# Optimization experiments

Measured on AMD Instinct MI355X. Metric: run time of the kernel, lower is better.

Reference implementation:

```python
import jax, jax.numpy as jnp
import numpy as np

B, T, D, DI, K, M, H, HD, L, VOCAB = 8, 512, 256, 512, 4, 2, 4, 64, 2, 272


def rmsnorm(x, w, eps=1e-6):
    return x * jax.lax.rsqrt(jnp.mean(x * x, axis=-1, keepdims=True) + eps) * w


def rotate_half(x):
    x1, x2 = x[..., ::2], x[..., 1::2]
    return jnp.stack([-x2, x1], axis=-1).reshape(x.shape)


def causal_conv(x, w, b):
    # x: [B,T,C], w: [C,K] depthwise causal conv, then silu
    y = jax.lax.conv_general_dilated(
        x.transpose(0, 2, 1), w[:, None, :],
        window_strides=(1,), padding=[(K - 1, 0)],
        feature_group_count=x.shape[-1])
    return jax.nn.silu(y.transpose(0, 2, 1) + b)


def delta_memory(x, Wv, Wg, Wb, Wa, A_log, dt_bias, Wblend, Wout):
    # x: [B,T,D]; per-timestep delta-rule fast-weight update with decay + key rotation
    Bv, Tn, Dm = x.shape
    vals = (x @ Wv).reshape(Bv, Tn, M, H, HD)
    gate = jax.nn.sigmoid(x @ Wg)                                   # [B,T,H]
    beta = jax.nn.sigmoid(jnp.einsum('btd,mdh->btmh', x, Wb))       # [B,T,M,H]
    alpha = jnp.einsum('btd,mdh->btmh', x, Wa) + dt_bias            # [B,T,M,H]
    decay = jnp.exp(-jnp.exp(A_log)[None, None] * jax.nn.softplus(alpha))
    blend = jax.nn.softmax((x @ Wblend).reshape(Bv, Tn, H, M), axis=-1)
    rk0 = x.reshape(Bv, Tn, H, HD)
    rk0 = rk0 / jnp.maximum(jnp.linalg.norm(rk0, axis=-1, keepdims=True), 1e-12)
    rks = [rk0]
    for _ in range(M - 1):
        rks.append(rotate_half(rks[-1]))
    rks = jnp.stack(rks, axis=2)                                    # [B,T,M,H,d]
    wks = jnp.pad(rks[:, :-1], ((0, 0), (1, 0), (0, 0), (0, 0), (0, 0)))  # shifted keys

    def step(S, inp):
        v, wk, rk, bt, dc, bl, g = inp
        S = S * dc[..., None, None]                                  # [B,M,H,d,d]
        pred = jnp.einsum('bmhdk,bmhd->bmhk', S, wk)
        err = (v - pred) * bt[..., None]
        S = S + wk[..., None] * err[..., None, :]                    # outer-product write
        read = jnp.einsum('bmhdk,bmhd->bmhk', S, rk)
        o = jnp.einsum('bhm,bmhk->bhk', bl, read) * g[..., None]
        return S, o

    tf = lambda a: jnp.moveaxis(a, 1, 0)
    xs = (tf(vals), tf(wks), tf(rks), tf(beta), tf(decay), tf(blend), tf(gate))
    S0 = jnp.zeros((Bv, M, H, HD, HD), x.dtype)
    _, o = jax.lax.scan(step, S0, xs)                                # [T,B,H,d]
    o = jnp.moveaxis(o, 0, 1).reshape(Bv, Tn, Dm)
    return x + o @ Wout


def setup_inputs():
    key = jax.random.key(0)
    ks = jax.random.split(key, 16)
    n = lambda k, shape, sc=0.02: jax.random.normal(k, shape, jnp.float32) * sc
    return {
        'ids': jax.random.randint(ks[0], (B, T), 0, VOCAB, jnp.int32),
        'emb': n(ks[1], (VOCAB, D)),
        'norm_w': jnp.ones((L, D), jnp.float32),
        'W_up': n(ks[2], (L, D, DI)),
        'W_gate': n(ks[3], (L, D, DI)),
        'W_down': n(ks[4], (L, DI, D)),
        'conv_w': n(ks[5], (L, DI, K), 0.1),
        'conv_b': jnp.zeros((L, DI), jnp.float32),
        'Wv': n(ks[6], (L, D, M * D)),
        'Wg': n(ks[7], (L, D, H)),
        'Wb': n(ks[8], (L, M, D, H)),
        'Wa': n(ks[9], (L, M, D, H)),
        'A_log': n(ks[10], (L, M, H), 0.5),
        'dt_bias': n(ks[11], (L, M, H), 0.5),
        'Wblend': n(ks[12], (L, D, H * M)),
        'Wout': n(ks[13], (L, D, D)),
        'final_norm_w': jnp.ones((D,), jnp.float32),
    }


def reference(ids, emb, norm_w, W_up, W_gate, W_down, conv_w, conv_b,
              Wv, Wg, Wb, Wa, A_log, dt_bias, Wblend, Wout, final_norm_w):
    x = emb[ids]
    for l in range(L):
        nx = rmsnorm(x, norm_w[l])
        h = causal_conv(nx @ W_up[l], conv_w[l], conv_b[l])
        out = (jax.nn.silu(nx @ W_gate[l]) * h) @ W_down[l]
        out = delta_memory(out, Wv[l], Wg[l], Wb[l], Wa[l],
                           A_log[l], dt_bias[l], Wblend[l], Wout[l])
        x = x + out
    return rmsnorm(x, final_norm_w) @ emb.T  # tied head
```

## Files before the change

### kernel.cpp

```cpp
#include <hip/hip_runtime.h>
#include <math.h>

#define BB 8
#define TT 512
#define DD 256
#define DIM 512
#define KW 4
#define MM 2
#define HH 4
#define HDIM 64
#define LL 2
#define VV 272

typedef __attribute__((ext_vector_type(8))) short bf16x8;
typedef __attribute__((ext_vector_type(4))) float f32x4;

__device__ __forceinline__ float sigf(float x){ return 1.f/(1.f+__expf(-x)); }
__device__ __forceinline__ float siluf(float x){ return x/(1.f+__expf(-x)); }

__device__ __forceinline__ unsigned short f2bf(float f){
  unsigned int u = __float_as_uint(f);
  unsigned int r = (u + 0x7FFFu + ((u >> 16) & 1u)) >> 16;
  return (unsigned short)r;
}
__device__ __forceinline__ float bf2f(unsigned short s){
  return __uint_as_float(((unsigned int)s) << 16);
}

__device__ __forceinline__ float xor1_add(float x){
  int y = __builtin_amdgcn_update_dpp(0, __float_as_int(x), 0xB1, 0xF, 0xF, true);
  return x + __int_as_float(y);
}
__device__ __forceinline__ float xor2_add(float x){
  int y = __builtin_amdgcn_update_dpp(0, __float_as_int(x), 0x4E, 0xF, 0xF, true);
  return x + __int_as_float(y);
}
__device__ __forceinline__ float xor8_add(float x){
  int y = __builtin_amdgcn_update_dpp(0, __float_as_int(x), 0x128, 0xF, 0xF, true);
  return x + __int_as_float(y);
}
__device__ __forceinline__ float ror4_add(float x){
  int y = __builtin_amdgcn_update_dpp(0, __float_as_int(x), 0x124, 0xF, 0xF, true);
  return x + __int_as_float(y);
}
__device__ __forceinline__ float ror8_add(float x){
  int y = __builtin_amdgcn_update_dpp(0, __float_as_int(x), 0x128, 0xF, 0xF, true);
  return x + __int_as_float(y);
}

__device__ __forceinline__ void gl_lds16(const void* g, void* l){
  __builtin_amdgcn_global_load_lds(
      (const __attribute__((address_space(1))) unsigned int*)g,
      (__attribute__((address_space(3))) unsigned int*)l,
      16, 0, 0);
}

#define LWB 589824
__global__ void k_cvt(const float* __restrict__ Wup, const float* __restrict__ Wgate,
                      const float* __restrict__ Wdown, const float* __restrict__ Wv,
                      const float* __restrict__ Wout, const float* __restrict__ emb,
                      unsigned short* __restrict__ wbf){
  int idx = blockIdx.x*256 + threadIdx.x;
  if (idx >= 2*LWB + VV*DD) return;
  float v;
  if (idx < 2*LWB){
    int l = (idx >= LWB) ? 1 : 0;
    int local = idx - l*LWB;
    if (local < 131072){ int n = local>>8, k = local&255;
      v = Wup[(size_t)l*131072 + k*DIM + n]; }
    else if (local < 262144){ local -= 131072; int n = local>>8, k = local&255;
      v = Wgate[(size_t)l*131072 + k*DIM + n]; }
    else if (local < 393216){ local -= 262144; int n = local>>9, k = local&511;
      v = Wdown[(size_t)l*131072 + k*DD + n]; }
    else if (local < 524288){ local -= 393216; int n = local>>8, k = local&255;
      v = Wv[(size_t)l*131072 + k*DIM + n]; }
    else { local -= 524288; int n = local>>8, k = local&255;
      v = Wout[(size_t)l*65536 + k*DD + n]; }
  } else {
    v = emb[idx - 2*LWB];
  }
  wbf[idx] = f2bf(v);
}

__global__ void k_embed(const int* __restrict__ ids, const float* __restrict__ emb,
                        float* __restrict__ x){
  int row = blockIdx.x;
  int d = threadIdx.x;
  x[row*DD + d] = emb[ids[row]*DD + d];
}

__global__ void k_rmsnorm(const float* __restrict__ in, const float* __restrict__ w,
                          unsigned short* __restrict__ out){
  int row = blockIdx.x;
  int l = threadIdx.x;
  float4 v = *(const float4*)&in[row*DD + l*4];
  float ss = v.x*v.x + v.y*v.y + v.z*v.z + v.w*v.w;
  #pragma unroll
  for (int o = 32; o > 0; o >>= 1) ss += __shfl_xor(ss, o, 64);
  float sc = rsqrtf(ss*(1.f/DD) + 1e-6f);
  float4 wv = *(const float4*)&w[l*4];
  ushort4 r;
  r.x = f2bf(v.x*sc*wv.x); r.y = f2bf(v.y*sc*wv.y);
  r.z = f2bf(v.z*sc*wv.z); r.w = f2bf(v.w*sc*wv.w);
  *(ushort4*)&out[row*DD + l*4] = r;
}

template<int MODE>
__global__ void __launch_bounds__(256) k_gemm2(const unsigned short* __restrict__ A,
                                               const unsigned short* __restrict__ Bt,
                                               float* __restrict__ Cf,
                                               unsigned short* __restrict__ Cb,
                                               int N, int K){
  __shared__ unsigned short as[64][72];
  __shared__ unsigned short bs[64][72];
  const int tid = threadIdx.x;
  const int w = tid >> 6, l = tid & 63;
  const int m0 = blockIdx.y*64, n0 = blockIdx.x*64;
  const int ar = tid >> 2, ac = (tid & 3)*16;
  f32x4 acc[4] = {};
  for (int k0 = 0; k0 < K; k0 += 64){
    { const bf16x8* src = (const bf16x8*)&A[(size_t)(m0+ar)*K + k0 + ac];
      *(bf16x8*)&as[ar][ac]   = src[0];
      *(bf16x8*)&as[ar][ac+8] = src[1];
    }
    { int n = n0 + ar;
      bf16x8 z; z = (bf16x8)(short)0;
      bf16x8 b0 = z, b1 = z;
      if (n < N){
        const bf16x8* src = (const bf16x8*)&Bt[(size_t)n*K + k0 + ac];
        b0 = src[0]; b1 = src[1];
      }
      *(bf16x8*)&bs[ar][ac]   = b0;
      *(bf16x8*)&bs[ar][ac+8] = b1;
    }
    __syncthreads();
    const int mr = w*16 + (l & 15);
    const int kb = (l >> 4)*8;
    #pragma unroll
    for (int kc2 = 0; kc2 < 2; ++kc2){
      bf16x8 af = *(const bf16x8*)&as[mr][kc2*32 + kb];
      #pragma unroll
      for (int nt = 0; nt < 4; ++nt){
        bf16x8 bfr = *(const bf16x8*)&bs[nt*16 + (l & 15)][kc2*32 + kb];
        acc[nt] = __builtin_amdgcn_mfma_f32_16x16x32_bf16(af, bfr, acc[nt], 0, 0, 0);
      }
    }
    __syncthreads();
  }
  #pragma unroll
  for (int nt = 0; nt < 4; ++nt){
    int col = n0 + nt*16 + (l & 15);
    if (col < N){
      #pragma unroll
      for (int r = 0; r < 4; ++r){
        int row = m0 + w*16 + (l >> 4)*4 + r;
        if (MODE == 0 || MODE == 2) Cf[(size_t)row*N + col] = acc[nt][r];
        if (MODE == 1 || MODE == 2) Cb[(size_t)row*N + col] = f2bf(acc[nt][r]);
      }
    }
  }
}

__global__ void __launch_bounds__(256) k_gemm_up(const unsigned short* __restrict__ A,
                                                 const unsigned short* __restrict__ But,
                                                 const unsigned short* __restrict__ Bgt,
                                                 unsigned short* __restrict__ Cu,
                                                 unsigned short* __restrict__ Cg){
  __shared__ unsigned short as[64][72];
  __shared__ unsigned short bu[64][72];
  __shared__ unsigned short bg[64][72];
  const int tid = threadIdx.x;
  const int w = tid >> 6, l = tid & 63;
  const int m0 = blockIdx.y*64, n0 = blockIdx.x*64;
  const int ar = tid >> 2, ac = (tid & 3)*16;
  f32x4 accu[4] = {}; f32x4 accg[4] = {};
  for (int k0 = 0; k0 < DD; k0 += 64){
    { const bf16x8* src = (const bf16x8*)&A[(size_t)(m0+ar)*DD + k0 + ac];
      *(bf16x8*)&as[ar][ac]   = src[0];
      *(bf16x8*)&as[ar][ac+8] = src[1];
    }
    { const bf16x8* s0 = (const bf16x8*)&But[(size_t)(n0+ar)*DD + k0 + ac];
      *(bf16x8*)&bu[ar][ac]   = s0[0];
      *(bf16x8*)&bu[ar][ac+8] = s0[1];
      const bf16x8* s1 = (const bf16x8*)&Bgt[(size_t)(n0+ar)*DD + k0 + ac];
      *(bf16x8*)&bg[ar][ac]   = s1[0];
      *(bf16x8*)&bg[ar][ac+8] = s1[1];
    }
    __syncthreads();
    const int mr = w*16 + (l & 15);
    const int kb = (l >> 4)*8;
    #pragma unroll
    for (int kc2 = 0; kc2 < 2; ++kc2){
      bf16x8 af = *(const bf16x8*)&as[mr][kc2*32 + kb];
      #pragma unroll
      for (int nt = 0; nt < 4; ++nt){
        bf16x8 b0 = *(const bf16x8*)&bu[nt*16 + (l & 15)][kc2*32 + kb];
        accu[nt] = __builtin_amdgcn_mfma_f32_16x16x32_bf16(af, b0, accu[nt], 0, 0, 0);
        bf16x8 b1 = *(const bf16x8*)&bg[nt*16 + (l & 15)][kc2*32 + kb];
        accg[nt] = __builtin_amdgcn_mfma_f32_16x16x32_bf16(af, b1, accg[nt], 0, 0, 0);
      }
    }
    __syncthreads();
  }
  #pragma unroll
  for (int nt = 0; nt < 4; ++nt){
    int col = n0 + nt*16 + (l & 15);
    #pragma unroll
    for (int r = 0; r < 4; ++r){
      int row = m0 + w*16 + (l >> 4)*4 + r;
      Cu[(size_t)row*DIM + col] = f2bf(accu[nt][r]);
      Cg[(size_t)row*DIM + col] = f2bf(accg[nt][r]);
    }
  }
}

__global__ void __launch_bounds__(256) k_gemm_wout(const float* __restrict__ p0,
                                                   const float* __restrict__ p1,
                                                   const unsigned short* __restrict__ Bt,
                                                   const float* __restrict__ y,
                                                   float* __restrict__ x){
  __shared__ unsigned short as[64][72];
  __shared__ unsigned short bs[64][72];
  const int tid = threadIdx.x;
  const int w = tid >> 6, l = tid & 63;
  const int m0 = blockIdx.y*64, n0 = blockIdx.x*64;
  const int ar = tid >> 2, ac = (tid & 3)*16;
  f32x4 acc[4] = {};
  for (int k0 = 0; k0 < DD; k0 += 64){
    #pragma unroll
    for (int j = 0; j < 4; ++j){
      size_t off = (size_t)(m0+ar)*DD + k0 + ac + j*4;
      float4 a = *(const float4*)&p0[off];
      float4 b = *(const float4*)&p1[off];
      a.x += b.x; a.y += b.y; a.z += b.z; a.w += b.w;
      ushort4 u = make_ushort4(f2bf(a.x), f2bf(a.y), f2bf(a.z), f2bf(a.w));
      *(ushort4*)&as[ar][ac + j*4] = u;
    }
    { const bf16x8* src = (const bf16x8*)&Bt[(size_t)(n0+ar)*DD + k0 + ac];
      *(bf16x8*)&bs[ar][ac]   = src[0];
      *(bf16x8*)&bs[ar][ac+8] = src[1];
    }
    __syncthreads();
    const int mr = w*16 + (l & 15);
    const int kb = (l >> 4)*8;
    #pragma unroll
    for (int kc2 = 0; kc2 < 2; ++kc2){
      bf16x8 af = *(const bf16x8*)&as[mr][kc2*32 + kb];
      #pragma unroll
      for (int nt = 0; nt < 4; ++nt){
        bf16x8 bfr = *(const bf16x8*)&bs[nt*16 + (l & 15)][kc2*32 + kb];
        acc[nt] = __builtin_amdgcn_mfma_f32_16x16x32_bf16(af, bfr, acc[nt], 0, 0, 0);
      }
    }
    __syncthreads();
  }
  #pragma unroll
  for (int nt = 0; nt < 4; ++nt){
    int col = n0 + nt*16 + (l & 15);
    #pragma unroll
    for (int r = 0; r < 4; ++r){
      int row = m0 + w*16 + (l >> 4)*4 + r;
      size_t off = (size_t)row*DD + col;
      x[off] = x[off] + y[off] + acc[nt][r];
    }
  }
}

__global__ void k_conv(const unsigned short* __restrict__ u,
                       const unsigned short* __restrict__ g,
                       const float* __restrict__ cw, const float* __restrict__ cb,
                       unsigned short* __restrict__ hh){
  int i8 = blockIdx.x*256 + threadIdx.x;
  int cg = i8 & 63;
  int bt = i8 >> 6;
  int t  = bt & (TT-1);
  int c0 = cg*8;
  float acc[8];
  { float4 b0 = *(const float4*)&cb[c0];
    float4 b1 = *(const float4*)&cb[c0+4];
    acc[0]=b0.x; acc[1]=b0.y; acc[2]=b0.z; acc[3]=b0.w;
    acc[4]=b1.x; acc[5]=b1.y; acc[6]=b1.z; acc[7]=b1.w; }
  float wts[8][4];
  #pragma unroll
  for (int i = 0; i < 8; ++i) *(float4*)&wts[i][0] = *(const float4*)&cw[(c0+i)*KW];
  #pragma unroll
  for (int j = 0; j < KW; ++j){
    int dt_ = j - (KW-1);
    if (t + dt_ >= 0){
      bf16x8 uv = *(const bf16x8*)&u[(size_t)(bt + dt_)*DIM + c0];
      #pragma unroll
      for (int i = 0; i < 8; ++i)
        acc[i] = fmaf(bf2f((unsigned short)uv[i]), wts[i][j], acc[i]);
    }
  }
  bf16x8 gv = *(const bf16x8*)&g[(size_t)bt*DIM + c0];
  bf16x8 o;
  #pragma unroll
  for (int i = 0; i < 8; ++i){
    float h = siluf(acc[i]);
    o[i] = (short)f2bf(siluf(bf2f((unsigned short)gv[i])) * h);
  }
  *(bf16x8*)&hh[(size_t)bt*DIM + c0] = o;
}

__global__ void __launch_bounds__(256) k_fused(const float* __restrict__ y,
    const float* __restrict__ Wg, const float* __restrict__ Wb,
    const float* __restrict__ Wa, const float* __restrict__ Wbl,
    const float* __restrict__ A_log, const float* __restrict__ dtb,
    float* __restrict__ rkb, float* __restrict__ scal){
  __shared__ float s_y[4][260];
  __shared__ float s_p[4][32];
  const int wv = threadIdx.x >> 6, l = threadIdx.x & 63;
  const int row = blockIdx.x*4 + wv;

  float4 yv = *(const float4*)&y[(size_t)row*DD + l*4];
  *(float4*)&s_y[wv][l*4] = yv;

  float ss = yv.x*yv.x + yv.y*yv.y + yv.z*yv.z + yv.w*yv.w;
  ss = xor1_add(ss); ss = xor2_add(ss);
  ss = ror4_add(ss); ss = ror8_add(ss);
  float inv = 1.f / fmaxf(sqrtf(ss), 1e-12f);
  float4 rv; rv.x = yv.x*inv; rv.y = yv.y*inv; rv.z = yv.z*inv; rv.w = yv.w*inv;
  *(float4*)&rkb[(size_t)row*DD + l*4] = rv;

  __syncthreads();

  const int j = (l < 28) ? l : 27;
  const float* wp; int stride;
  if (j < 4){ wp = Wg + j; stride = HH; }
  else if (j < 12){ int m=(j-4)>>2, h=(j-4)&3; wp = Wb + (size_t)m*DD*HH + h; stride = HH; }
  else if (j < 20){ int m=(j-12)>>2, h=(j-12)&3; wp = Wa + (size_t)m*DD*HH + h; stride = HH; }
  else { wp = Wbl + (j-20); stride = HH*MM; }
  float a0=0.f,a1=0.f,a2=0.f,a3=0.f;
  #pragma unroll 4
  for (int k = 0; k < DD; k += 4){
    a0 = fmaf(s_y[wv][k+0], wp[(k+0)*stride], a0);
    a1 = fmaf(s_y[wv][k+1], wp[(k+1)*stride], a1);
    a2 = fmaf(s_y[wv][k+2], wp[(k+2)*stride], a2);
    a3 = fmaf(s_y[wv][k+3], wp[(k+3)*stride], a3);
  }
  if (l < 28) s_p[wv][l] = (a0+a1)+(a2+a3);

  __syncthreads();

  if (l < 8){
    int m = l >> 2, h = l & 3;
    float gs  = sigf(s_p[wv][h]);
    float btv = sigf(s_p[wv][4 + m*4 + h]);
    float sp  = s_p[wv][12 + m*4 + h] + dtb[m*HH + h];
    sp = (sp > 15.f) ? sp : log1pf(__expf(sp));
    float dc  = __expf(-__expf(A_log[m*HH + h]) * sp);
    float l0 = s_p[wv][20 + h*2], l1 = s_p[wv][20 + h*2 + 1];
    float mx = fmaxf(l0, l1);
    float e0 = __expf(l0-mx), e1 = __expf(l1-mx);
    float bl = (m ? e1 : e0) / (e0 + e1);
    float4 o; o.x = dc; o.y = btv; o.z = bl*gs; o.w = 0.f;
    *(float4*)&scal[((size_t)row*MM + m)*(HH*4) + h*4] = o;
  }
}


#define SSTEP(T_, WK, RK, PF, VB, SB) { \
  const float dc = SB.x, btv = SB.y, blg = SB.z; \
  const float v = VB; \
  { const int tn_ = ((T_)+2 < 64) ? (T_)+2 : 63; \
    PF[0] = *(const float4*)&s_rk[p][tn_][dbase + 0]; \
    PF[1] = *(const float4*)&s_rk[p][tn_][dbase + 4]; \
    VB = bf2f(s_v[p][tn_][klocal]); \
    SB = *(const float4*)&s_sc[p][tn_][0]; } \
  const float err = (v - dc*rrc)*btv; \
  float rr0=0.f,rr1=0.f; \
  _Pragma("unroll") \
  for (int jj = 0; jj < 2; ++jj){ const float4 rp = WK[jj]; const float4 rc = RK[jj]; \
    float w0,w1,w2,w3,c0,c1,c2,c3; \
    if (ROT == 0){ w0=rp.x; w1=rp.y; w2=rp.z; w3=rp.w; c0=rc.x; c1=rc.y; c2=rc.z; c3=rc.w; } \
    else { w0=-rp.y; w1=rp.x; w2=-rp.w; w3=rp.z; c0=-rc.y; c1=rc.x; c2=-rc.w; c3=rc.z; } \
    S[4*jj+0] = fmaf(S[4*jj+0], dc, w0*err); rr0 = fmaf(S[4*jj+0], c0, rr0); \
    S[4*jj+1] = fmaf(S[4*jj+1], dc, w1*err); rr1 = fmaf(S[4*jj+1], c1, rr1); \
    S[4*jj+2] = fmaf(S[4*jj+2], dc, w2*err); rr0 = fmaf(S[4*jj+2], c2, rr0); \
    S[4*jj+3] = fmaf(S[4*jj+3], dc, w3*err); rr1 = fmaf(S[4*jj+3], c3, rr1); } \
  float rr = rr0 + rr1; \
  rr = xor1_add(rr); rr = xor2_add(rr); rr = xor8_add(rr); \
  rrc = rr; \
  if (q == 0) part[(size_t)(rowchunk + (T_))*DD + h*HDIM + kq*8 + klocal] = blg*rr; \
}

template<int ROT>
__device__ __forceinline__ void scan_body(int b, int h, int kq, int l,
    const unsigned short* __restrict__ vals, const float* __restrict__ rkb,
    const float* __restrict__ scal, float* __restrict__ part,
    float (*s_rk)[64][64], unsigned short (*s_v)[64][8], float (*s_sc)[64][4])
{
  const int q = (l & 3) | ((l & 8) >> 1);
  const int klocal = ((l >> 2) & 1) | ((l >> 3) & 6);
  const int dbase = q*8;
  const int rowbase = b*TT;

  float S[8];
  #pragma unroll
  for (int j = 0; j < 8; ++j) S[j] = 0.f;
  const float4 Z = make_float4(0.f,0.f,0.f,0.f);
  float4 rb0[2]={Z,Z}, rb1[2]={Z,Z}, rb2[2]={Z,Z}, rb3[2]={Z,Z};
  float vb0 = 0.f, vb1 = 0.f;
  float4 sb0 = Z, sb1 = Z;
  float rrc = 0.f;

  auto stage = [&](int c, int pbuf){
    const int r0 = rowbase + c*64;
    #pragma unroll
    for (int i = 0; i < 16; ++i){
      const float* g = rkb + (size_t)(r0 + i*4 + (l>>4))*DD + h*HDIM + (l&15)*4;
      gl_lds16(g, &s_rk[pbuf][i*4][0]);
    }
    { const unsigned short* g = vals + ((size_t)(r0 + l)*MM + ROT)*DD + h*HDIM + kq*8;
      gl_lds16(g, &s_v[pbuf][0][0]); }
    { const float* g = scal + ((size_t)(r0 + l)*MM + ROT)*(HH*4) + h*4;
      gl_lds16(g, &s_sc[pbuf][0][0]); }
  };

  stage(0, 0);
  for (int c = 0; c < TT/64; ++c){
    const int p = c & 1;
    __syncthreads();
    if (c + 1 < TT/64) stage(c+1, p^1);
    rb0[0] = *(const float4*)&s_rk[p][0][dbase]; rb0[1] = *(const float4*)&s_rk[p][0][dbase+4];
    rb1[0] = *(const float4*)&s_rk[p][1][dbase]; rb1[1] = *(const float4*)&s_rk[p][1][dbase+4];
    vb0 = bf2f(s_v[p][0][klocal]); vb1 = bf2f(s_v[p][1][klocal]);
    sb0 = *(const float4*)&s_sc[p][0][0]; sb1 = *(const float4*)&s_sc[p][1][0];
    const int rowchunk = rowbase + c*64;
    for (int tt = 0; tt < 64; tt += 4){
      SSTEP(tt+0, rb3, rb0, rb2, vb0, sb0)
      SSTEP(tt+1, rb0, rb1, rb3, vb1, sb1)
      SSTEP(tt+2, rb1, rb2, rb0, vb0, sb0)
      SSTEP(tt+3, rb2, rb3, rb1, vb1, sb1)
    }
  }
}

__global__ void __launch_bounds__(64) k_scan(const unsigned short* __restrict__ vals,
                                             const float* __restrict__ rkb,
                                             const float* __restrict__ scal,
                                             float* __restrict__ partials){
  __shared__ float s_rk[2][64][64];
  __shared__ unsigned short s_v[2][64][8];
  __shared__ float s_sc[2][64][4];
  const int bi = blockIdx.x;
  const int kq = bi & 7;
  const int m  = (bi >> 3) & 1;
  const int h  = (bi >> 4) & 3;
  const int b  = bi >> 6;
  float* part = partials + (size_t)m*(BB*TT*DD);
  if (m == 0) scan_body<0>(b, h, kq, threadIdx.x, vals, rkb, scal, part, s_rk, s_v, s_sc);
  else        scan_body<1>(b, h, kq, threadIdx.x, vals, rkb, scal, part, s_rk, s_v, s_sc);
}

extern "C" void kernel_launch(void* const* d_in, const int* in_sizes, int n_in,
                              void* d_out, int out_size, void* d_ws, size_t ws_size,
                              hipStream_t stream){
  const int*   ids   = (const int*)d_in[0];
  const float* emb   = (const float*)d_in[1];
  const float* normw = (const float*)d_in[2];
  const float* Wup   = (const float*)d_in[3];
  const float* Wgate = (const float*)d_in[4];
  const float* Wdown = (const float*)d_in[5];
  const float* convw = (const float*)d_in[6];
  const float* convb = (const float*)d_in[7];
  const float* Wv    = (const float*)d_in[8];
  const float* Wg    = (const float*)d_in[9];
  const float* Wb    = (const float*)d_in[10];
  const float* Wa    = (const float*)d_in[11];
  const float* A_log = (const float*)d_in[12];
  const float* dtb   = (const float*)d_in[13];
  const float* Wbl   = (const float*)d_in[14];
  const float* Wout  = (const float*)d_in[15];
  const float* fnw   = (const float*)d_in[16];
  float* out = (float*)d_out;

  const int ROWS = BB*TT;
  const size_t MEG = 1u << 20;
  float* ws   = (float*)d_ws;
  float* x    = ws;
  unsigned short* nyb = (unsigned short*)(x + MEG);
  float* big1 = x + MEG + MEG/2;
  float* big2 = big1 + 2*MEG;
  float* y    = big2 + 2*MEG;
  float* rkb  = y    + MEG;
  float* scal = rkb  + MEG;
  unsigned short* wbf = (unsigned short*)(scal + (1u<<17));

  unsigned short* ub  = (unsigned short*)big1;
  unsigned short* gb  = (unsigned short*)(big1 + MEG);
  unsigned short* valsb = ub;

  { int total = 2*LWB + VV*DD;
    k_cvt<<<(total + 255)/256, 256, 0, stream>>>(Wup, Wgate, Wdown, Wv, Wout, emb, wbf); }

  k_embed<<<ROWS, DD, 0, stream>>>(ids, emb, x);

  for (int l = 0; l < LL; ++l){
    unsigned short* wl = wbf + (size_t)l*LWB;
    unsigned short* upT   = wl;
    unsigned short* gateT = wl + 131072;
    unsigned short* downT = wl + 262144;
    unsigned short* wvT   = wl + 393216;
    unsigned short* woutT = wl + 524288;

    k_rmsnorm<<<ROWS, 64, 0, stream>>>(x, normw + l*DD, nyb);
    k_gemm_up<<<dim3(DIM/64, ROWS/64), 256, 0, stream>>>(nyb, upT, gateT, ub, gb);
    k_conv<<<(ROWS*DIM/8)/256, 256, 0, stream>>>(ub, gb, convw + l*DIM*KW, convb + l*DIM, gb);
    k_gemm2<2><<<dim3(DD/64, ROWS/64), 256, 0, stream>>>(gb, downT, y, nyb, DD, DIM);
    k_gemm2<1><<<dim3(DIM/64, ROWS/64), 256, 0, stream>>>(nyb, wvT, nullptr, valsb, DIM, DD);
    k_fused<<<ROWS/4, 256, 0, stream>>>(y, Wg + l*DD*HH, Wb + (size_t)l*MM*DD*HH,
                                        Wa + (size_t)l*MM*DD*HH, Wbl + l*DD*HH*MM,
                                        A_log + l*MM*HH, dtb + l*MM*HH, rkb, scal);
    k_scan<<<BB*HH*MM*8, 64, 0, stream>>>(valsb, rkb, scal, big2);
    k_gemm_wout<<<dim3(DD/64, ROWS/64), 256, 0, stream>>>(big2, big2 + MEG, woutT, y, x);
  }

  unsigned short* embT = wbf + 2*LWB;
  k_rmsnorm<<<ROWS, 64, 0, stream>>>(x, fnw, nyb);
  k_gemm2<0><<<dim3((VV+63)/64, ROWS/64), 256, 0, stream>>>(nyb, embT, out, nullptr, VV, DD);
}
```

Measured before the change: 295.9 us.

## Enlarge GEMM tiles to 128 rows and split scan state across twice the blocks

GEMM kernels now compute 128x64 output tiles, each wave holding two 16-row MFMA accumulator sets, which reduces B-tile reloads but halves the grid. The delta-rule scan kernel halves per-lane state from 8 to 4 elements, using 16 lanes per key column and twice as many blocks, to shorten the serial per-timestep critical path. This adds an extra DPP reduction stage and duplicates staging of rk and scalar data across blocks. The smaller GEMM grids may underfill the GPU.

```diff
diff --git a/kernel.cpp b/kernel.cpp
--- a/kernel.cpp
+++ b/kernel.cpp
@@ -33,10 +33,6 @@
 }
 __device__ __forceinline__ float xor2_add(float x){
   int y = __builtin_amdgcn_update_dpp(0, __float_as_int(x), 0x4E, 0xF, 0xF, true);
-  return x + __int_as_float(y);
-}
-__device__ __forceinline__ float xor8_add(float x){
-  int y = __builtin_amdgcn_update_dpp(0, __float_as_int(x), 0x128, 0xF, 0xF, true);
   return x + __int_as_float(y);
 }
 __device__ __forceinline__ float ror4_add(float x){
@@ -111,51 +107,59 @@
                                                float* __restrict__ Cf,
                                                unsigned short* __restrict__ Cb,
                                                int N, int K){
-  __shared__ unsigned short as[64][72];
+  __shared__ unsigned short as[128][72];
   __shared__ unsigned short bs[64][72];
   const int tid = threadIdx.x;
   const int w = tid >> 6, l = tid & 63;
-  const int m0 = blockIdx.y*64, n0 = blockIdx.x*64;
-  const int ar = tid >> 2, ac = (tid & 3)*16;
-  f32x4 acc[4] = {};
+  const int m0 = blockIdx.y*128, n0 = blockIdx.x*64;
+  const int ar = tid >> 1, ac = (tid & 1)*32;
+  const int br = tid >> 2, bc = (tid & 3)*16;
+  f32x4 acc[2][4] = {};
   for (int k0 = 0; k0 < K; k0 += 64){
     { const bf16x8* src = (const bf16x8*)&A[(size_t)(m0+ar)*K + k0 + ac];
-      *(bf16x8*)&as[ar][ac]   = src[0];
-      *(bf16x8*)&as[ar][ac+8] = src[1];
-    }
-    { int n = n0 + ar;
+      *(bf16x8*)&as[ar][ac]    = src[0];
+      *(bf16x8*)&as[ar][ac+8]  = src[1];
+      *(bf16x8*)&as[ar][ac+16] = src[2];
+      *(bf16x8*)&as[ar][ac+24] = src[3];
+    }
+    { int n = n0 + br;
       bf16x8 z; z = (bf16x8)(short)0;
       bf16x8 b0 = z, b1 = z;
       if (n < N){
-        const bf16x8* src = (const bf16x8*)&Bt[(size_t)n*K + k0 + ac];
-        b0 = src[0]; b1 = src[1];
-      }
-      *(bf16x8*)&bs[ar][ac]   = b0;
-      *(bf16x8*)&bs[ar][ac+8] = b1;
-    }
-    __syncthreads();
-    const int mr = w*16 + (l & 15);
-    const int kb = (l >> 4)*8;
+        const bf16x8* s = (const bf16x8*)&Bt[(size_t)n*K + k0 + bc];
+        b0 = s[0]; b1 = s[1];
+      }
+      *(bf16x8*)&bs[br][bc]   = b0;
+      *(bf16x8*)&bs[br][bc+8] = b1;
+    }
+    __syncthreads();
+    const int lr = l & 15, kb = (l >> 4)*8;
     #pragma unroll
     for (int kc2 = 0; kc2 < 2; ++kc2){
-      bf16x8 af = *(const bf16x8*)&as[mr][kc2*32 + kb];
+      bf16x8 af0 = *(const bf16x8*)&as[w*32 + lr][kc2*32 + kb];
+      bf16x8 af1 = *(const bf16x8*)&as[w*32 + 16 + lr][kc2*32 + kb];
       #pragma unroll
       for (int nt = 0; nt < 4; ++nt){
-        bf16x8 bfr = *(const bf16x8*)&bs[nt*16 + (l & 15)][kc2*32 + kb];
-        acc[nt] = __builtin_amdgcn_mfma_f32_16x16x32_bf16(af, bfr, acc[nt], 0, 0, 0);
-      }
-    }
-    __syncthreads();
-  }
-  #pragma unroll
-  for (int nt = 0; nt < 4; ++nt){
-    int col = n0 + nt*16 + (l & 15);
-    if (col < N){
-      #pragma unroll
-      for (int r = 0; r < 4; ++r){
-        int row = m0 + w*16 + (l >> 4)*4 + r;
-        if (MODE == 0 || MODE == 2) Cf[(size_t)row*N + col] = acc[nt][r];
-        if (MODE == 1 || MODE == 2) Cb[(size_t)row*N + col] = f2bf(acc[nt][r]);
+        bf16x8 bfr = *(const bf16x8*)&bs[nt*16 + lr][kc2*32 + kb];
+        acc[0][nt] = __builtin_amdgcn_mfma_f32_16x16x32_bf16(af0, bfr, acc[0][nt], 0, 0, 0);
+        acc[1][nt] = __builtin_amdgcn_mfma_f32_16x16x32_bf16(af1, bfr, acc[1][nt], 0, 0, 0);
+      }
+    }
+    __syncthreads();
+  }
+  const int lr = l & 15;
+  #pragma unroll
+  for (int mt = 0; mt < 2; ++mt){
+    #pragma unroll
+    for (int nt = 0; nt < 4; ++nt){
+      int col = n0 + nt*16 + lr;
+      if (col < N){
+        #pragma unroll
+        for (int r = 0; r < 4; ++r){
+          int row = m0 + w*32 + mt*16 + (l >> 4)*4 + r;
+          if (MODE == 0 || MODE == 2) Cf[(size_t)row*N + col] = acc[mt][nt][r];
+          if (MODE == 1 || MODE == 2) Cb[(size_t)row*N + col] = f2bf(acc[mt][nt][r]);
+        }
       }
     }
   }
@@ -166,50 +170,59 @@
                                                  const unsigned short* __restrict__ Bgt,
                                                  unsigned short* __restrict__ Cu,
                                                  unsigned short* __restrict__ Cg){
-  __shared__ unsigned short as[64][72];
+  __shared__ unsigned short as[128][72];
   __shared__ unsigned short bu[64][72];
   __shared__ unsigned short bg[64][72];
   const int tid = threadIdx.x;
   const int w = tid >> 6, l = tid & 63;
-  const int m0 = blockIdx.y*64, n0 = blockIdx.x*64;
-  const int ar = tid >> 2, ac = (tid & 3)*16;
-  f32x4 accu[4] = {}; f32x4 accg[4] = {};
+  const int m0 = blockIdx.y*128, n0 = blockIdx.x*64;
+  const int ar = tid >> 1, ac = (tid & 1)*32;
+  const int br = tid >> 2, bc = (tid & 3)*16;
+  f32x4 accu[2][4] = {}; f32x4 accg[2][4] = {};
   for (int k0 = 0; k0 < DD; k0 += 64){
     { const bf16x8* src = (const bf16x8*)&A[(size_t)(m0+ar)*DD + k0 + ac];
-      *(bf16x8*)&as[ar][ac]   = src[0];
-      *(bf16x8*)&as[ar][ac+8] = src[1];
-    }
-    { const bf16x8* s0 = (const bf16x8*)&But[(size_t)(n0+ar)*DD + k0 + ac];
-      *(bf16x8*)&bu[ar][ac]   = s0[0];
-      *(bf16x8*)&bu[ar][ac+8] = s0[1];
-      const bf16x8* s1 = (const bf16x8*)&Bgt[(size_t)(n0+ar)*DD + k0 + ac];
-      *(bf16x8*)&bg[ar][ac]   = s1[0];
-      *(bf16x8*)&bg[ar][ac+8] = s1[1];
-    }
-    __syncthreads();
-    const int mr = w*16 + (l & 15);
-    const int kb = (l >> 4)*8;
+      *(bf16x8*)&as[ar][ac]    = src[0];
+      *(bf16x8*)&as[ar][ac+8]  = src[1];
+      *(bf16x8*)&as[ar][ac+16] = src[2];
+      *(bf16x8*)&as[ar][ac+24] = src[3];
+    }
+    { const bf16x8* s0 = (const bf16x8*)&But[(size_t)(n0+br)*DD + k0 + bc];
+      *(bf16x8*)&bu[br][bc]   = s0[0];
+      *(bf16x8*)&bu[br][bc+8] = s0[1];
+      const bf16x8* s1 = (const bf16x8*)&Bgt[(size_t)(n0+br)*DD + k0 + bc];
+      *(bf16x8*)&bg[br][bc]   = s1[0];
+      *(bf16x8*)&bg[br][bc+8] = s1[1];
+    }
+    __syncthreads();
+    const int lr = l & 15, kb = (l >> 4)*8;
     #pragma unroll
     for (int kc2 = 0; kc2 < 2; ++kc2){
-      bf16x8 af = *(const bf16x8*)&as[mr][kc2*32 + kb];
+      bf16x8 af0 = *(const bf16x8*)&as[w*32 + lr][kc2*32 + kb];
+      bf16x8 af1 = *(const bf16x8*)&as[w*32 + 16 + lr][kc2*32 + kb];
       #pragma unroll
       for (int nt = 0; nt < 4; ++nt){
-        bf16x8 b0 = *(const bf16x8*)&bu[nt*16 + (l & 15)][kc2*32 + kb];
-        accu[nt] = __builtin_amdgcn_mfma_f32_16x16x32_bf16(af, b0, accu[nt], 0, 0, 0);
-        bf16x8 b1 = *(const bf16x8*)&bg[nt*16 + (l & 15)][kc2*32 + kb];
-        accg[nt] = __builtin_amdgcn_mfma_f32_16x16x32_bf16(af, b1, accg[nt], 0, 0, 0);
-      }
-    }
-    __syncthreads();
-  }
-  #pragma unroll
-  for (int nt = 0; nt < 4; ++nt){
-    int col = n0 + nt*16 + (l & 15);
-    #pragma unroll
-    for (int r = 0; r < 4; ++r){
-      int row = m0 + w*16 + (l >> 4)*4 + r;
-      Cu[(size_t)row*DIM + col] = f2bf(accu[nt][r]);
-      Cg[(size_t)row*DIM + col] = f2bf(accg[nt][r]);
+        bf16x8 b0 = *(const bf16x8*)&bu[nt*16 + lr][kc2*32 + kb];
+        accu[0][nt] = __builtin_amdgcn_mfma_f32_16x16x32_bf16(af0, b0, accu[0][nt], 0, 0, 0);
+        accu[1][nt] = __builtin_amdgcn_mfma_f32_16x16x32_bf16(af1, b0, accu[1][nt], 0, 0, 0);
+        bf16x8 b1 = *(const bf16x8*)&bg[nt*16 + lr][kc2*32 + kb];
+        accg[0][nt] = __builtin_amdgcn_mfma_f32_16x16x32_bf16(af0, b1, accg[0][nt], 0, 0, 0);
+        accg[1][nt] = __builtin_amdgcn_mfma_f32_16x16x32_bf16(af1, b1, accg[1][nt], 0, 0, 0);
+      }
+    }
+    __syncthreads();
+  }
+  const int lr = l & 15;
+  #pragma unroll
+  for (int mt = 0; mt < 2; ++mt){
+    #pragma unroll
+    for (int nt = 0; nt < 4; ++nt){
+      int col = n0 + nt*16 + lr;
+      #pragma unroll
+      for (int r = 0; r < 4; ++r){
+        int row = m0 + w*32 + mt*16 + (l >> 4)*4 + r;
+        Cu[(size_t)row*DIM + col] = f2bf(accu[mt][nt][r]);
+        Cg[(size_t)row*DIM + col] = f2bf(accg[mt][nt][r]);
+      }
     }
   }
 }
@@ -219,16 +232,17 @@
                                                    const unsigned short* __restrict__ Bt,
                                                    const float* __restrict__ y,
                                                    float* __restrict__ x){
-  __shared__ unsigned short as[64][72];
+  __shared__ unsigned short as[128][72];
   __shared__ unsigned short bs[64][72];
   const int tid = threadIdx.x;
   const int w = tid >> 6, l = tid & 63;
-  const int m0 = blockIdx.y*64, n0 = blockIdx.x*64;
-  const int ar = tid >> 2, ac = (tid & 3)*16;
-  f32x4 acc[4] = {};
+  const int m0 = blockIdx.y*128, n0 = blockIdx.x*64;
+  const int ar = tid >> 1, ac = (tid & 1)*32;
+  const int br = tid >> 2, bc = (tid & 3)*16;
+  f32x4 acc[2][4] = {};
   for (int k0 = 0; k0 < DD; k0 += 64){
     #pragma unroll
-    for (int j = 0; j < 4; ++j){
+    for (int j = 0; j < 8; ++j){
       size_t off = (size_t)(m0+ar)*DD + k0 + ac + j*4;
       float4 a = *(const float4*)&p0[off];
       float4 b = *(const float4*)&p1[off];
@@ -236,32 +250,37 @@
       ushort4 u = make_ushort4(f2bf(a.x), f2bf(a.y), f2bf(a.z), f2bf(a.w));
       *(ushort4*)&as[ar][ac + j*4] = u;
     }
-    { const bf16x8* src = (const bf16x8*)&Bt[(size_t)(n0+ar)*DD + k0 + ac];
-      *(bf16x8*)&bs[ar][ac]   = src[0];
-      *(bf16x8*)&bs[ar][ac+8] = src[1];
-    }
-    __syncthreads();
-    const int mr = w*16 + (l & 15);
-    const int kb = (l >> 4)*8;
+    { const bf16x8* src = (const bf16x8*)&Bt[(size_t)(n0+br)*DD + k0 + bc];
+      *(bf16x8*)&bs[br][bc]   = src[0];
+      *(bf16x8*)&bs[br][bc+8] = src[1];
+    }
+    __syncthreads();
+    const int lr = l & 15, kb = (l >> 4)*8;
     #pragma unroll
     for (int kc2 = 0; kc2 < 2; ++kc2){
-      bf16x8 af = *(const bf16x8*)&as[mr][kc2*32 + kb];
+      bf16x8 af0 = *(const bf16x8*)&as[w*32 + lr][kc2*32 + kb];
+      bf16x8 af1 = *(const bf16x8*)&as[w*32 + 16 + lr][kc2*32 + kb];
       #pragma unroll
       for (int nt = 0; nt < 4; ++nt){
-        bf16x8 bfr = *(const bf16x8*)&bs[nt*16 + (l & 15)][kc2*32 + kb];
-        acc[nt] = __builtin_amdgcn_mfma_f32_16x16x32_bf16(af, bfr, acc[nt], 0, 0, 0);
-      }
-    }
-    __syncthreads();
-  }
-  #pragma unroll
-  for (int nt = 0; nt < 4; ++nt){
-    int col = n0 + nt*16 + (l & 15);
-    #pragma unroll
-    for (int r = 0; r < 4; ++r){
-      int row = m0 + w*16 + (l >> 4)*4 + r;
-      size_t off = (size_t)row*DD + col;
-      x[off] = x[off] + y[off] + acc[nt][r];
+        bf16x8 bfr = *(const bf16x8*)&bs[nt*16 + lr][kc2*32 + kb];
+        acc[0][nt] = __builtin_amdgcn_mfma_f32_16x16x32_bf16(af0, bfr, acc[0][nt], 0, 0, 0);
+        acc[1][nt] = __builtin_amdgcn_mfma_f32_16x16x32_bf16(af1, bfr, acc[1][nt], 0, 0, 0);
+      }
+    }
+    __syncthreads();
+  }
+  const int lr = l & 15;
+  #pragma unroll
+  for (int mt = 0; mt < 2; ++mt){
+    #pragma unroll
+    for (int nt = 0; nt < 4; ++nt){
+      int col = n0 + nt*16 + lr;
+      #pragma unroll
+      for (int r = 0; r < 4; ++r){
+        int row = m0 + w*32 + mt*16 + (l >> 4)*4 + r;
+        size_t off = (size_t)row*DD + col;
+        x[off] = x[off] + y[off] + acc[mt][nt][r];
+      }
     }
   }
 }
@@ -364,43 +383,42 @@
   const float dc = SB.x, btv = SB.y, blg = SB.z; \
   const float v = VB; \
   { const int tn_ = ((T_)+2 < 64) ? (T_)+2 : 63; \
-    PF[0] = *(const float4*)&s_rk[p][tn_][dbase + 0]; \
-    PF[1] = *(const float4*)&s_rk[p][tn_][dbase + 4]; \
-    VB = bf2f(s_v[p][tn_][klocal]); \
+    PF = *(const float4*)&s_rk[p][tn_][dbase]; \
+    VB = bf2f(s_v[p][tn_][vidx]); \
     SB = *(const float4*)&s_sc[p][tn_][0]; } \
   const float err = (v - dc*rrc)*btv; \
-  float rr0=0.f,rr1=0.f; \
-  _Pragma("unroll") \
-  for (int jj = 0; jj < 2; ++jj){ const float4 rp = WK[jj]; const float4 rc = RK[jj]; \
+  float rr0=0.f, rr1=0.f; \
+  { const float4 rp = WK; const float4 rc = RK; \
     float w0,w1,w2,w3,c0,c1,c2,c3; \
     if (ROT == 0){ w0=rp.x; w1=rp.y; w2=rp.z; w3=rp.w; c0=rc.x; c1=rc.y; c2=rc.z; c3=rc.w; } \
     else { w0=-rp.y; w1=rp.x; w2=-rp.w; w3=rp.z; c0=-rc.y; c1=rc.x; c2=-rc.w; c3=rc.z; } \
-    S[4*jj+0] = fmaf(S[4*jj+0], dc, w0*err); rr0 = fmaf(S[4*jj+0], c0, rr0); \
-    S[4*jj+1] = fmaf(S[4*jj+1], dc, w1*err); rr1 = fmaf(S[4*jj+1], c1, rr1); \
-    S[4*jj+2] = fmaf(S[4*jj+2], dc, w2*err); rr0 = fmaf(S[4*jj+2], c2, rr0); \
-    S[4*jj+3] = fmaf(S[4*jj+3], dc, w3*err); rr1 = fmaf(S[4*jj+3], c3, rr1); } \
+    S[0] = fmaf(S[0], dc, w0*err); rr0 = fmaf(S[0], c0, rr0); \
+    S[1] = fmaf(S[1], dc, w1*err); rr1 = fmaf(S[1], c1, rr1); \
+    S[2] = fmaf(S[2], dc, w2*err); rr0 = fmaf(S[2], c2, rr0); \
+    S[3] = fmaf(S[3], dc, w3*err); rr1 = fmaf(S[3], c3, rr1); } \
   float rr = rr0 + rr1; \
-  rr = xor1_add(rr); rr = xor2_add(rr); rr = xor8_add(rr); \
+  rr = xor1_add(rr); rr = xor2_add(rr); rr = ror4_add(rr); rr = ror8_add(rr); \
   rrc = rr; \
-  if (q == 0) part[(size_t)(rowchunk + (T_))*DD + h*HDIM + kq*8 + klocal] = blg*rr; \
+  if (seg == 0) part[(size_t)(rowchunk + (T_))*DD + h*HDIM + kq4*4 + klocal] = blg*rr; \
 }
 
 template<int ROT>
-__device__ __forceinline__ void scan_body(int b, int h, int kq, int l,
+__device__ __forceinline__ void scan_body(int b, int h, int kq4, int l,
     const unsigned short* __restrict__ vals, const float* __restrict__ rkb,
     const float* __restrict__ scal, float* __restrict__ part,
     float (*s_rk)[64][64], unsigned short (*s_v)[64][8], float (*s_sc)[64][4])
 {
-  const int q = (l & 3) | ((l & 8) >> 1);
-  const int klocal = ((l >> 2) & 1) | ((l >> 3) & 6);
-  const int dbase = q*8;
+  const int seg = l & 15, klocal = l >> 4;
+  const int dbase = seg*4;
+  const int vidx = (kq4 & 1)*4 + klocal;
+  const int kq8 = kq4 >> 1;
   const int rowbase = b*TT;
 
-  float S[8];
-  #pragma unroll
-  for (int j = 0; j < 8; ++j) S[j] = 0.f;
+  float S[4];
+  #pragma unroll
+  for (int j = 0; j < 4; ++j) S[j] = 0.f;
   const float4 Z = make_float4(0.f,0.f,0.f,0.f);
-  float4 rb0[2]={Z,Z}, rb1[2]={Z,Z}, rb2[2]={Z,Z}, rb3[2]={Z,Z};
+  float4 rb0 = Z, rb1 = Z, rb2 = Z, rb3 = Z;
   float vb0 = 0.f, vb1 = 0.f;
   float4 sb0 = Z, sb1 = Z;
   float rrc = 0.f;
@@ -412,7 +430,7 @@
       const float* g = rkb + (size_t)(r0 + i*4 + (l>>4))*DD + h*HDIM + (l&15)*4;
       gl_lds16(g, &s_rk[pbuf][i*4][0]);
     }
-    { const unsigned short* g = vals + ((size_t)(r0 + l)*MM + ROT)*DD + h*HDIM + kq*8;
+    { const unsigned short* g = vals + ((size_t)(r0 + l)*MM + ROT)*DD + h*HDIM + kq8*8;
       gl_lds16(g, &s_v[pbuf][0][0]); }
     { const float* g = scal + ((size_t)(r0 + l)*MM + ROT)*(HH*4) + h*4;
       gl_lds16(g, &s_sc[pbuf][0][0]); }
@@ -423,9 +441,9 @@
     const int p = c & 1;
     __syncthreads();
     if (c + 1 < TT/64) stage(c+1, p^1);
-    rb0[0] = *(const float4*)&s_rk[p][0][dbase]; rb0[1] = *(const float4*)&s_rk[p][0][dbase+4];
-    rb1[0] = *(const float4*)&s_rk[p][1][dbase]; rb1[1] = *(const float4*)&s_rk[p][1][dbase+4];
-    vb0 = bf2f(s_v[p][0][klocal]); vb1 = bf2f(s_v[p][1][klocal]);
+    rb0 = *(const float4*)&s_rk[p][0][dbase];
+    rb1 = *(const float4*)&s_rk[p][1][dbase];
+    vb0 = bf2f(s_v[p][0][vidx]); vb1 = bf2f(s_v[p][1][vidx]);
     sb0 = *(const float4*)&s_sc[p][0][0]; sb1 = *(const float4*)&s_sc[p][1][0];
     const int rowchunk = rowbase + c*64;
     for (int tt = 0; tt < 64; tt += 4){
@@ -445,13 +463,13 @@
   __shared__ unsigned short s_v[2][64][8];
   __shared__ float s_sc[2][64][4];
   const int bi = blockIdx.x;
-  const int kq = bi & 7;
-  const int m  = (bi >> 3) & 1;
-  const int h  = (bi >> 4) & 3;
-  const int b  = bi >> 6;
+  const int kq4 = bi & 15;
+  const int m  = (bi >> 4) & 1;
+  const int h  = (bi >> 5) & 3;
+  const int b  = bi >> 7;
   float* part = partials + (size_t)m*(BB*TT*DD);
-  if (m == 0) scan_body<0>(b, h, kq, threadIdx.x, vals, rkb, scal, part, s_rk, s_v, s_sc);
-  else        scan_body<1>(b, h, kq, threadIdx.x, vals, rkb, scal, part, s_rk, s_v, s_sc);
+  if (m == 0) scan_body<0>(b, h, kq4, threadIdx.x, vals, rkb, scal, part, s_rk, s_v, s_sc);
+  else        scan_body<1>(b, h, kq4, threadIdx.x, vals, rkb, scal, part, s_rk, s_v, s_sc);
 }
 
 extern "C" void kernel_launch(void* const* d_in, const int* in_sizes, int n_in,
@@ -506,18 +524,18 @@
     unsigned short* woutT = wl + 524288;
 
     k_rmsnorm<<<ROWS, 64, 0, stream>>>(x, normw + l*DD, nyb);
-    k_gemm_up<<<dim3(DIM/64, ROWS/64), 256, 0, stream>>>(nyb, upT, gateT, ub, gb);
+    k_gemm_up<<<dim3(DIM/64, ROWS/128), 256, 0, stream>>>(nyb, upT, gateT, ub, gb);
     k_conv<<<(ROWS*DIM/8)/256, 256, 0, stream>>>(ub, gb, convw + l*DIM*KW, convb + l*DIM, gb);
-    k_gemm2<2><<<dim3(DD/64, ROWS/64), 256, 0, stream>>>(gb, downT, y, nyb, DD, DIM);
-    k_gemm2<1><<<dim3(DIM/64, ROWS/64), 256, 0, stream>>>(nyb, wvT, nullptr, valsb, DIM, DD);
+    k_gemm2<2><<<dim3(DD/64, ROWS/128), 256, 0, stream>>>(gb, downT, y, nyb, DD, DIM);
+    k_gemm2<1><<<dim3(DIM/64, ROWS/128), 256, 0, stream>>>(nyb, wvT, nullptr, valsb, DIM, DD);
     k_fused<<<ROWS/4, 256, 0, stream>>>(y, Wg + l*DD*HH, Wb + (size_t)l*MM*DD*HH,
                                         Wa + (size_t)l*MM*DD*HH, Wbl + l*DD*HH*MM,
                                         A_log + l*MM*HH, dtb + l*MM*HH, rkb, scal);
-    k_scan<<<BB*HH*MM*8, 64, 0, stream>>>(valsb, rkb, scal, big2);
-    k_gemm_wout<<<dim3(DD/64, ROWS/64), 256, 0, stream>>>(big2, big2 + MEG, woutT, y, x);
+    k_scan<<<BB*HH*MM*16, 64, 0, stream>>>(valsb, rkb, scal, big2);
+    k_gemm_wout<<<dim3(DD/64, ROWS/128), 256, 0, stream>>>(big2, big2 + MEG, woutT, y, x);
   }
 
   unsigned short* embT = wbf + 2*LWB;
   k_rmsnorm<<<ROWS, 64, 0, stream>>>(x, fnw, nyb);
-  k_gemm2<0><<<dim3((VV+63)/64, ROWS/64), 256, 0, stream>>>(nyb, embT, out, nullptr, VV, DD);
-}
+  k_gemm2<0><<<dim3((VV+63)/64, ROWS/128), 256, 0, stream>>>(nyb, embT, out, nullptr, VV, DD);
+}
```

Result: slower. 306.2 us (+3.5%).
